# Performance work log

Hardware: AMD Instinct MI355X
Metric: run time of the kernel (lower is better)

Reference implementation:

```python
import jax, jax.numpy as jnp
import numpy as np

L, B, D, H, R, C, WIN = 256, 64, 1024, 512, 8, 6, 10
N = B * L
DH = D + H  # concat(node_features, graph output)


def _window_pairs():
    pi, pk = [], []
    for j in range(L):
        for k in range(max(0, j - WIN), min(L, j + WIN + 1)):
            pi.append(j)
            pk.append(k)
    return np.asarray(pi, np.int32), np.asarray(pk, np.int32)


def setup_inputs() -> dict:
    key = jax.random.key(0)
    ks = jax.random.split(key, 16)
    s = 0.02
    pi, pk = _window_pairs()
    return {
        "features": jax.random.normal(ks[0], (L, B, D), jnp.float32),
        "Wscalar": jax.random.normal(ks[1], (D, L), jnp.float32) * s,   # MaskedEdgeAttention scalar
        "W_rel": jax.random.normal(ks[2], (R, D, H), jnp.float32) * s,  # RGCN per-relation weights
        "W_root": jax.random.normal(ks[3], (D, H), jnp.float32) * s,
        "b_rgcn": jnp.zeros((H,), jnp.float32),
        "W_nbr": jax.random.normal(ks[4], (H, H), jnp.float32) * s,     # GraphConv neighbor weight
        "W_self": jax.random.normal(ks[5], (H, H), jnp.float32) * s,
        "b_gc": jnp.zeros((H,), jnp.float32),
        "W_match": jax.random.normal(ks[6], (DH, DH), jnp.float32) * s,  # MatchingAttention 'general2'
        "b_match": jnp.zeros((DH,), jnp.float32),
        "W_lin": jax.random.normal(ks[7], (DH, H), jnp.float32) * s,
        "b_lin": jnp.zeros((H,), jnp.float32),
        "W_fc": jax.random.normal(ks[8], (H, C), jnp.float32) * s,
        "b_fc": jnp.zeros((C,), jnp.float32),
        "speakers": jax.random.randint(ks[9], (L, B), 0, 2, jnp.int32),
        "pair_i": jnp.asarray(pi),
        "pair_k": jnp.asarray(pk),
    }


def reference(features, Wscalar, W_rel, W_root, b_rgcn, W_nbr, W_self, b_gc,
              W_match, b_match, W_lin, b_lin, W_fc, b_fc,
              speakers, pair_i, pair_k):
    # --- edge attention scores (MaskedEdgeAttention, attn1 style) ---
    scale = jnp.einsum('sbd,dm->sbm', features, Wscalar)      # [L,B,L]
    alpha = jax.nn.softmax(scale, axis=0)
    alpha = jnp.transpose(alpha, (1, 2, 0))                   # [B, anchor, src]
    win = jnp.full((L, L), 1e-10, jnp.float32).at[pair_i, pair_k].set(1.0)
    masked = alpha * win
    scores = masked / jnp.sum(masked, axis=-1, keepdims=True)  # renormalized over window
    edge_norm = scores[:, pair_i, pair_k].reshape(-1)          # [E]

    # --- batch_graphify: flatten nodes conversation-major, build global edges ---
    x = jnp.transpose(features, (1, 0, 2)).reshape(N, D)       # [N, D]
    offs = jnp.arange(B, dtype=jnp.int32)[:, None] * L
    src = (offs + pair_i[None, :]).reshape(-1)
    dst = (offs + pair_k[None, :]).reshape(-1)
    sp = speakers.T                                            # [B, L]
    dir_bit = jnp.where(pair_i < pair_k, 0, 1).astype(jnp.int32)
    rel = (sp[:, pair_i] * 4 + sp[:, pair_k] * 2 + dir_bit[None, :]).reshape(-1)

    # --- RGCNConv: per-relation transform, edge_norm-weighted sum at dst + root ---
    h_all = jnp.einsum('nd,rdh->nrh', x, W_rel)                # [N, R, H]
    msg = h_all[src, rel] * edge_norm[:, None]                 # [E, H]
    agg = jax.ops.segment_sum(msg, dst, num_segments=N)
    h1 = agg + x @ W_root + b_rgcn

    # --- GraphConv: W_nbr @ sum_j x_j + W_self @ x + b ---
    nbr = jax.ops.segment_sum(h1[src], dst, num_segments=N)
    h2 = nbr @ W_nbr + h1 @ W_self + b_gc

    # --- attentive_node_features (MatchingAttention 'general2', full-length mask=1) ---
    em = jnp.concatenate([x, h2], axis=-1).reshape(B, L, DH)
    em = jnp.transpose(em, (1, 0, 2))                          # [L, B, DH] seq-major
    xt = jnp.einsum('tbd,de->tbe', em, W_match) + b_match
    a = jax.nn.softmax(jnp.tanh(jnp.einsum('tbe,sbe->bts', xt, em)), axis=2)
    att = jnp.einsum('bts,sbd->tbd', a, em)                    # [L, B, DH]

    # --- classify_node_features (dropout = eval identity) ---
    hidden = jax.nn.relu(jnp.einsum('tbd,dh->tbh', att, W_lin) + b_lin)
    logp = jax.nn.log_softmax(hidden @ W_fc + b_fc, axis=2)    # [L, B, C]
    return jnp.transpose(logp, (1, 0, 2)).reshape(N, C)
```

## Files before the change

### kernel.cpp

```cpp
#include <hip/hip_runtime.h>
#include <hip/hip_bf16.h>

#define Lc 256
#define Bc 64
#define Dc 1024
#define Hc 512
#define Rc 8
#define Cc 6
#define WINc 10
#define NWc 21
#define Nc (Bc*Lc)
#define DHc (Dc+Hc)
#define CH 8192

typedef __attribute__((ext_vector_type(8))) short short8;
typedef __attribute__((ext_vector_type(4))) float floatx4;

__device__ inline unsigned short f2b(float x) {
    __hip_bfloat16 h = __float2bfloat16(x);
    return *reinterpret_cast<unsigned short*>(&h);
}
__device__ inline float bf2f(unsigned short u) {
    __hip_bfloat16 h;
    *reinterpret_cast<unsigned short*>(&h) = u;
    return __bfloat162float(h);
}

__device__ inline long remap_row(int node) { return (long)(((node & 255) << 6) + (node >> 8)); }

typedef __attribute__((address_space(3))) unsigned int lds_u32;
typedef __attribute__((address_space(1))) unsigned int glb_u32;
__device__ inline void glds16(const unsigned short* g, unsigned short* l) {
    __builtin_amdgcn_global_load_lds((const glb_u32*)g, (lds_u32*)l, 16, 0, 0);
}

#define SB0 __builtin_amdgcn_sched_barrier(0)
#define BAR __builtin_amdgcn_s_barrier()

__device__ __forceinline__ void xcd_remap(int gridX, int& x, int& y)
{
    int nwg = gridDim.x * gridDim.y;
    int bid = blockIdx.y * gridDim.x + blockIdx.x;
    int q = nwg >> 3, r = nwg & 7;
    int xcd = bid & 7, pos = bid >> 3;
    int logical = xcd * q + min(xcd, r) + pos;
    x = logical % gridX;
    y = logical / gridX;
}

__global__ __launch_bounds__(256) void transpose_all(
    const float* __restrict__ Wscalar, const float* __restrict__ W_rel,
    const float* __restrict__ W_root, const float* __restrict__ W_nbr,
    const float* __restrict__ W_self, const float* __restrict__ W_match,
    const float* __restrict__ W_lin, unsigned short* __restrict__ WT)
{
    int t = blockIdx.x;
    const float* in; unsigned short* out; int N, ldo, n0, k0;
    if (t < 256) {
        in = Wscalar; out = WT; N = 256; ldo = 1024;
        n0 = (t & 7) * 32; k0 = (t >> 3) * 32;
    } else if (t < 4352) {
        int u = t - 256; int r = u >> 9; u &= 511;
        in = W_rel + (long)r * 524288; out = WT + 262144 + (long)r * 524288; N = 512; ldo = 1024;
        n0 = (u & 15) * 32; k0 = (u >> 4) * 32;
    } else if (t < 4864) {
        int u = t - 4352;
        in = W_root; out = WT + 262144 + 4096 * 1024; N = 512; ldo = 1024;
        n0 = (u & 15) * 32; k0 = (u >> 4) * 32;
    } else if (t < 5120) {
        int u = t - 4864;
        in = W_nbr; out = WT + 4980736; N = 512; ldo = 1024;
        n0 = (u & 15) * 32; k0 = (u >> 4) * 32;
    } else if (t < 5376) {
        int u = t - 5120;
        in = W_self; out = WT + 4980736 + 512; N = 512; ldo = 1024;
        n0 = (u & 15) * 32; k0 = (u >> 4) * 32;
    } else if (t < 7680) {
        int u = t - 5376;
        in = W_match; out = WT + 5505024; N = 1536; ldo = 1536;
        n0 = (u % 48) * 32; k0 = (u / 48) * 32;
    } else {
        int u = t - 7680;
        in = W_lin; out = WT + 7864320; N = 512; ldo = 1536;
        n0 = (u & 15) * 32; k0 = (u >> 4) * 32;
    }
    __shared__ float tt[32][33];
    int tx = threadIdx.x & 31, ty = threadIdx.x >> 5;
    #pragma unroll
    for (int i = 0; i < 4; i++) tt[ty + i * 8][tx] = in[(long)(k0 + ty + i * 8) * N + n0 + tx];
    __syncthreads();
    #pragma unroll
    for (int i = 0; i < 4; i++) out[(long)(n0 + ty + i * 8) * ldo + k0 + tx] = f2b(tt[tx][ty + i * 8]);
}

__global__ __launch_bounds__(256) void partition_kernel(const int* __restrict__ spk,
        int* __restrict__ idx, int* __restrict__ cnts)
{
    int c = blockIdx.x;
    int tid = threadIdx.x;
    int base = c * CH;
    __shared__ int zs[256];
    int zcount = 0;
    for (int i = 0; i < CH / 256; i++) {
        int n = base + tid * (CH / 256) + i;
        if (spk[(n & 255) * 64 + (n >> 8)] == 0) zcount++;
    }
    zs[tid] = zcount; __syncthreads();
    for (int off = 1; off < 256; off <<= 1) {
        int v = (tid >= off) ? zs[tid - off] : 0;
        __syncthreads();
        zs[tid] += v;
        __syncthreads();
    }
    int Z = zs[255];
    int zpos = zs[tid] - zcount;
    int opos = tid * (CH / 256) - zpos;
    for (int i = 0; i < CH / 256; i++) {
        int nl = tid * (CH / 256) + i;
        int n = base + nl;
        if (spk[(n & 255) * 64 + (n >> 8)] == 0) idx[base + (zpos++)] = nl;
        else                                     idx[base + Z + (opos++)] = nl;
    }
    if (tid == 0) cnts[c] = Z;
}

__global__ __launch_bounds__(256) void build_em_x(const float* __restrict__ feats,
                                                  unsigned short* __restrict__ em)
{
    int n = blockIdx.x;
    int tid = threadIdx.x;
    const float* f = feats + remap_row(n) * Dc;
    float4 v = ((const float4*)f)[tid];
    unsigned short* e = em + (long)n * DHc + tid * 4;
    e[0] = f2b(v.x); e[1] = f2b(v.y); e[2] = f2b(v.z); e[3] = f2b(v.w);
}

template<bool CBF, bool CT, bool BIAS, bool RELU>
__global__ __launch_bounds__(256) void gemm_as(
    const unsigned short* __restrict__ A, const unsigned short* __restrict__ B,
    void* __restrict__ Cv, const float* __restrict__ bias,
    int K, int lda, int ldb, int ldc, long sA, long sB, long sC)
{
    __shared__ __align__(16) unsigned short As[4096];
    __shared__ __align__(16) unsigned short Bs[4096];
    const int tid = threadIdx.x;
    const int z = blockIdx.z;
    const int m0 = blockIdx.y * 128, n0 = blockIdx.x * 128;
    const int lane = tid & 63, wave = tid >> 6;
    const int q = lane >> 4, mr = lane & 15;
    const int wrow = (wave >> 1) * 64, wcol = (wave & 1) * 64;

    const unsigned short* Ag0 = A + z * sA + (long)(m0 + wave * 32 + mr) * lda + q * 8;
    const unsigned short* Ag1 = Ag0 + (long)16 * lda;
    const unsigned short* Bg0 = B + z * sB + (long)(n0 + wave * 32 + mr) * ldb + q * 8;
    const unsigned short* Bg1 = Bg0 + (long)16 * ldb;
    unsigned short* Al0 = As + wave * 1024;
    unsigned short* Bl0 = Bs + wave * 1024;

    floatx4 acc[4][4];
    #pragma unroll
    for (int mt = 0; mt < 4; mt++)
        #pragma unroll
        for (int nt = 0; nt < 4; nt++) acc[mt][nt] = (floatx4){0.f, 0.f, 0.f, 0.f};

    const int ga = (wave >> 1) * 2048;
    const int gb = (wave & 1) * 2048;

    for (int k0 = 0; k0 < K; k0 += 32) {
        glds16(Ag0 + k0, Al0);
        glds16(Ag1 + k0, Al0 + 512);
        glds16(Bg0 + k0, Bl0);
        glds16(Bg1 + k0, Bl0 + 512);
        __syncthreads();
        short8 af[4], bfr[4];
        #pragma unroll
        for (int t = 0; t < 4; t++) {
            af[t]  = *(const short8*)&As[ga + t * 512 + lane * 8];
            bfr[t] = *(const short8*)&Bs[gb + t * 512 + lane * 8];
        }
        #pragma unroll
        for (int mt = 0; mt < 4; mt++)
            #pragma unroll
            for (int nt = 0; nt < 4; nt++)
                acc[mt][nt] = __builtin_amdgcn_mfma_f32_16x16x32_bf16(af[mt], bfr[nt], acc[mt][nt], 0, 0, 0);
        __syncthreads();
    }

    float* Cf = (float*)Cv;
    unsigned short* Cb = (unsigned short*)Cv;
    #pragma unroll
    for (int mt = 0; mt < 4; mt++) {
        #pragma unroll
        for (int nt = 0; nt < 4; nt++) {
            int col = n0 + wcol + nt * 16 + mr;
            float bv = BIAS ? bias[col] : 0.f;
            #pragma unroll
            for (int rg = 0; rg < 4; rg++) {
                int row = m0 + wrow + mt * 16 + q * 4 + rg;
                float v = acc[mt][nt][rg] + bv;
                if (RELU) v = fmaxf(v, 0.f);
                if (CT) {
                    Cb[(long)(row >> 8) * 131072 + (long)col * 256 + (row & 255)] = f2b(v);
                } else {
                    long ci = z * sC + (long)row * ldc + col;
                    if (CBF) Cb[ci] = f2b(v);
                    else     Cf[ci] = v;
                }
            }
        }
    }
}

#define MFMA16(ACCBASE, AFR, BFR) \
    { _Pragma("unroll") \
      for (int mt = 0; mt < 4; mt++) \
        _Pragma("unroll") \
        for (int nt = 0; nt < 4; nt++) \
            acc[ACCBASE + mt][nt] = __builtin_amdgcn_mfma_f32_16x16x32_bf16(AFR[mt], BFR[nt], acc[ACCBASE + mt][nt], 0, 0, 0); }

__device__ __forceinline__ void gemm256_loop(
    unsigned short* lp,
    const unsigned short* Ag0, const unsigned short* Ag1,
    const unsigned short* Bg0, const unsigned short* Bg1,
    int NT, int wofs, const int* offA, const int* offB, floatx4 (&acc)[8][4])
{
    glds16(Ag0,      lp + wofs);                 glds16(Ag1,      lp + 4096 + wofs);
    glds16(Bg0,      lp + 32768 + wofs);         glds16(Bg1,      lp + 32768 + 4096 + wofs);
    glds16(Ag0 + 32, lp + 8192 + wofs);          glds16(Ag1 + 32, lp + 8192 + 4096 + wofs);
    glds16(Bg0 + 32, lp + 32768 + 8192 + wofs);  glds16(Bg1 + 32, lp + 32768 + 8192 + 4096 + wofs);
    glds16(Ag0 + 64, lp + 16384 + wofs);         glds16(Ag1 + 64, lp + 16384 + 4096 + wofs);
    glds16(Bg0 + 64, lp + 32768 + 16384 + wofs); glds16(Bg1 + 64, lp + 32768 + 16384 + 4096 + wofs);
    asm volatile("s_waitcnt vmcnt(4)" ::: "memory");
    SB0; BAR; SB0;

    short8 aQ[4], a2Q[4], bQ[4], b2Q[4];
    #pragma unroll
    for (int i = 0; i < 4; i++) aQ[i] = *(const short8*)(lp + offA[i]);
    #pragma unroll
    for (int i = 0; i < 4; i++) bQ[i] = *(const short8*)(lp + 32768 + offB[i]);

    for (int t = 0; t < NT; t++) {
        const int buf = t & 1;
        const int ab  = buf * 16384;

        if (t + 1 < NT) {
            const int kc = (t + 1) * 64 + 32;
            unsigned short* d = lp + (buf ^ 1) * 16384 + 8192 + wofs;
            glds16(Ag0 + kc, d); glds16(Ag1 + kc, d + 4096);
        }
        #pragma unroll
        for (int i = 0; i < 4; i++) a2Q[i] = *(const short8*)(lp + ab + offA[4 + i]);
        SB0; BAR; SB0;
        __builtin_amdgcn_s_setprio(1);
        MFMA16(0, aQ, bQ)
        __builtin_amdgcn_s_setprio(0);
        SB0; BAR; SB0;

        if (t + 1 < NT) {
            const int kc = (t + 1) * 64 + 32;
            unsigned short* d = lp + 32768 + (buf ^ 1) * 16384 + 8192 + wofs;
            glds16(Bg0 + kc, d); glds16(Bg1 + kc, d + 4096);
        }
        #pragma unroll
        for (int i = 0; i < 4; i++) aQ[i]  = *(const short8*)(lp + ab + 8192 + offA[i]);
        #pragma unroll
        for (int i = 0; i < 4; i++) b2Q[i] = *(const short8*)(lp + 32768 + ab + 8192 + offB[i]);
        SB0; BAR; SB0;
        __builtin_amdgcn_s_setprio(1);
        MFMA16(4, a2Q, bQ)
        __builtin_amdgcn_s_setprio(0);
        SB0; BAR; SB0;

        if (t + 2 < NT) {
            const int kc = (t + 2) * 64;
            unsigned short* d = lp + buf * 16384 + wofs;
            glds16(Ag0 + kc, d); glds16(Ag1 + kc, d + 4096);
        }
        #pragma unroll
        for (int i = 0; i < 4; i++) a2Q[i] = *(const short8*)(lp + ab + 8192 + offA[4 + i]);
        SB0; BAR; SB0;
        __builtin_amdgcn_s_setprio(1);
        MFMA16(0, aQ, b2Q)
        __builtin_amdgcn_s_setprio(0);
        SB0; BAR; SB0;

        if (t + 2 < NT) {
            const int kc = (t + 2) * 64;
            unsigned short* d = lp + 32768 + buf * 16384 + wofs;
            glds16(Bg0 + kc, d); glds16(Bg1 + kc, d + 4096);
        }
        if (t < NT - 2)       { asm volatile("s_waitcnt vmcnt(4)" ::: "memory"); }
        else if (t == NT - 2) { asm volatile("s_waitcnt vmcnt(0)" ::: "memory"); }
        SB0; BAR; SB0;
        if (t + 1 < NT) {
            const int ab2 = (buf ^ 1) * 16384;
            #pragma unroll
            for (int i = 0; i < 4; i++) aQ[i] = *(const short8*)(lp + ab2 + offA[i]);
            #pragma unroll
            for (int i = 0; i < 4; i++) bQ[i] = *(const short8*)(lp + 32768 + ab2 + offB[i]);
        }
        SB0;
        __builtin_amdgcn_s_setprio(1);
        MFMA16(4, a2Q, b2Q)
        __builtin_amdgcn_s_setprio(0);
        SB0; BAR; SB0;
    }
}

__device__ __forceinline__ void frag_offsets(int wm, int wn, int q, int mr, int* offA, int* offB)
{
    #pragma unroll
    for (int mt = 0; mt < 8; mt++) {
        int row = wm * 128 + mt * 16 + mr;
        offA[mt] = row * 32 + ((q ^ ((row >> 1) & 3)) * 8);
    }
    #pragma unroll
    for (int nt = 0; nt < 4; nt++) {
        int row = wn * 64 + nt * 16 + mr;
        offB[nt] = row * 32 + ((q ^ ((row >> 1) & 3)) * 8);
    }
}

template<bool CBF, bool CT, bool BIAS, bool RELU>
__global__ __launch_bounds__(512, 2) void gemm256(
    const unsigned short* __restrict__ A, const unsigned short* __restrict__ B,
    void* __restrict__ Cv, const float* __restrict__ bias,
    int K, int lda, int ldb, int ldc)
{
    __shared__ __align__(16) unsigned short LDS[65536];
    unsigned short* lp = &LDS[0];
    const int tid  = threadIdx.x;
    const int lane = tid & 63, wave = tid >> 6;
    const int wm = wave >> 2, wn = wave & 3;
    int bx, by;
    xcd_remap(gridDim.x, bx, by);
    const int m0 = by * 256, n0 = bx * 256;
    const int NT = K >> 6;
    const int q = lane >> 4, mr = lane & 15;

    const int r0 = wave * 16 + (lane >> 2);
    const int r1 = r0 + 128;
    const int c0 = ((lane & 3) ^ ((r0 >> 1) & 3)) * 8;
    const int c1 = ((lane & 3) ^ ((r1 >> 1) & 3)) * 8;
    const unsigned short* Ag0 = A + (long)(m0 + r0) * lda + c0;
    const unsigned short* Ag1 = A + (long)(m0 + r1) * lda + c1;
    const unsigned short* Bg0 = B + (long)(n0 + r0) * ldb + c0;
    const unsigned short* Bg1 = B + (long)(n0 + r1) * ldb + c1;
    const int wofs = wave * 512;

    int offA[8], offB[4];
    frag_offsets(wm, wn, q, mr, offA, offB);

    floatx4 acc[8][4];
    #pragma unroll
    for (int mt = 0; mt < 8; mt++)
        #pragma unroll
        for (int nt = 0; nt < 4; nt++) acc[mt][nt] = (floatx4){0.f, 0.f, 0.f, 0.f};

    gemm256_loop(lp, Ag0, Ag1, Bg0, Bg1, NT, wofs, offA, offB, acc);

    float* Cf = (float*)Cv;
    unsigned short* Cb = (unsigned short*)Cv;
    #pragma unroll
    for (int mt = 0; mt < 8; mt++) {
        #pragma unroll
        for (int nt = 0; nt < 4; nt++) {
            int col = n0 + wn * 64 + nt * 16 + mr;
            float bv = BIAS ? bias[col] : 0.f;
            #pragma unroll
            for (int rg = 0; rg < 4; rg++) {
                int row = m0 + wm * 128 + mt * 16 + q * 4 + rg;
                float v = acc[mt][nt][rg] + bv;
                if (RELU) v = fmaxf(v, 0.f);
                if (CT) {
                    Cb[(long)(row >> 8) * 131072 + (long)col * 256 + (row & 255)] = f2b(v);
                } else {
                    long ci = (long)row * ldc + col;
                    if (CBF) Cb[ci] = f2b(v);
                    else     Cf[ci] = v;
                }
            }
        }
    }
}

__global__ __launch_bounds__(512, 2) void rgcn256(
    const unsigned short* __restrict__ A, const unsigned short* __restrict__ B,
    unsigned short* __restrict__ C, const int* __restrict__ idx,
    const int* __restrict__ cntp)
{
    const int cnt0 = *cntp;
    const int t0 = (cnt0 + 255) >> 8;
    const int M1 = CH - cnt0;
    const int t1 = (M1 + 255) >> 8;
    int x, ty;
    xcd_remap(gridDim.x, x, ty);
    int sblk, m0, M, off;
    if (ty < t0)           { sblk = 0; m0 = ty << 8;        M = cnt0; off = 0; }
    else if (ty < t0 + t1) { sblk = 1; m0 = (ty - t0) << 8; M = M1;   off = cnt0; }
    else return;

    const int brow = ((x < 8) ? sblk * 2048 : 2048) + x * 256;

    __shared__ __align__(16) unsigned short LDS[65536];
    unsigned short* lp = &LDS[0];
    const int tid  = threadIdx.x;
    const int lane = tid & 63, wave = tid >> 6;
    const int wm = wave >> 2, wn = wave & 3;
    const int q = lane >> 4, mr = lane & 15;

    const int r0 = wave * 16 + (lane >> 2);
    const int r1 = r0 + 128;
    const int c0 = ((lane & 3) ^ ((r0 >> 1) & 3)) * 8;
    const int c1 = ((lane & 3) ^ ((r1 >> 1) & 3)) * 8;
    const int gr0 = idx[off + min(m0 + r0, M - 1)];
    const int gr1 = idx[off + min(m0 + r1, M - 1)];
    const unsigned short* Ag0 = A + (long)gr0 * DHc + c0;
    const unsigned short* Ag1 = A + (long)gr1 * DHc + c1;
    const unsigned short* Bg0 = B + (long)(brow + r0) * 1024 + c0;
    const unsigned short* Bg1 = B + (long)(brow + r1) * 1024 + c1;
    const int wofs = wave * 512;

    int offA[8], offB[4];
    frag_offsets(wm, wn, q, mr, offA, offB);

    floatx4 acc[8][4];
    #pragma unroll
    for (int mt = 0; mt < 8; mt++)
        #pragma unroll
        for (int nt = 0; nt < 4; nt++) acc[mt][nt] = (floatx4){0.f, 0.f, 0.f, 0.f};

    gemm256_loop(lp, Ag0, Ag1, Bg0, Bg1, 16 , wofs, offA, offB, acc);

    #pragma unroll
    for (int mt = 0; mt < 8; mt++) {
        int rowb = m0 + wm * 128 + mt * 16 + q * 4;
        int cr[4];
        #pragma unroll
        for (int rg = 0; rg < 4; rg++) cr[rg] = idx[off + min(rowb + rg, M - 1)];
        #pragma unroll
        for (int nt = 0; nt < 4; nt++) {
            int col = x * 256 + wn * 64 + nt * 16 + mr;
            #pragma unroll
            for (int rg = 0; rg < 4; rg++)
                C[(long)cr[rg] * 2560 + col] = f2b(acc[mt][nt][rg]);
        }
    }
}

__global__ __launch_bounds__(512, 2) void gemm256_mw(
    const unsigned short* __restrict__ A, const unsigned short* __restrict__ B,
    unsigned short* __restrict__ xt, unsigned short* __restrict__ emWT,
    const float* __restrict__ b_match, const float* __restrict__ b_lin)
{
    __shared__ __align__(16) unsigned short LDS[65536];
    unsigned short* lp = &LDS[0];
    const int tid  = threadIdx.x;
    const int lane = tid & 63, wave = tid >> 6;
    const int wm = wave >> 2, wn = wave & 3;
    int bx, by;
    xcd_remap(gridDim.x, bx, by);
    const int m0 = by * 256, n0 = bx * 256;
    const int q = lane >> 4, mr = lane & 15;

    const int r0 = wave * 16 + (lane >> 2);
    const int r1 = r0 + 128;
    const int c0 = ((lane & 3) ^ ((r0 >> 1) & 3)) * 8;
    const int c1 = ((lane & 3) ^ ((r1 >> 1) & 3)) * 8;
    const unsigned short* Ag0 = A + (long)(m0 + r0) * DHc + c0;
    const unsigned short* Ag1 = A + (long)(m0 + r1) * DHc + c1;
    const unsigned short* Bg0 = B + (long)(n0 + r0) * 1536 + c0;
    const unsigned short* Bg1 = B + (long)(n0 + r1) * 1536 + c1;
    const int wofs = wave * 512;

    int offA[8], offB[4];
    frag_offsets(wm, wn, q, mr, offA, offB);

    floatx4 acc[8][4];
    #pragma unroll
    for (int mt = 0; mt < 8; mt++)
        #pragma unroll
        for (int nt = 0; nt < 4; nt++) acc[mt][nt] = (floatx4){0.f, 0.f, 0.f, 0.f};

    gemm256_loop(lp, Ag0, Ag1, Bg0, Bg1, 24 , wofs, offA, offB, acc);

    if (n0 < 1536) {
        #pragma unroll
        for (int mt = 0; mt < 8; mt++) {
            #pragma unroll
            for (int nt = 0; nt < 4; nt++) {
                int col = n0 + wn * 64 + nt * 16 + mr;
                float bv = b_match[col];
                #pragma unroll
                for (int rg = 0; rg < 4; rg++) {
                    int row = m0 + wm * 128 + mt * 16 + q * 4 + rg;
                    xt[(long)row * DHc + col] = f2b(acc[mt][nt][rg] + bv);
                }
            }
        }
    } else {
        #pragma unroll
        for (int mt = 0; mt < 8; mt++) {
            #pragma unroll
            for (int nt = 0; nt < 4; nt++) {
                int col = (n0 - 1536) + wn * 64 + nt * 16 + mr;
                float bv = b_lin[col];
                #pragma unroll
                for (int rg = 0; rg < 4; rg++) {
                    int row = m0 + wm * 128 + mt * 16 + q * 4 + rg;
                    emWT[(long)(row >> 8) * 131072 + (long)col * 256 + (row & 255)] =
                        f2b(acc[mt][nt][rg] + bv);
                }
            }
        }
    }
}

__global__ __launch_bounds__(256) void edge_norm_kernel(const float* __restrict__ scale,
                                                        float* __restrict__ enorm)
{
    int g = blockIdx.x * 256 + threadIdx.x;
    int b = g >> 8, j = g & 255;
    int klo = max(0, j - WINc), khi = min(Lc - 1, j + WINc);
    float vals[NWc];
    float m = -1e30f;
    for (int k = klo; k <= khi; k++) {
        float v = scale[(long)((b << 8) + k) * Lc + j];
        vals[k - klo] = v;
        m = fmaxf(m, v);
    }
    float s = 0.f;
    for (int k = klo; k <= khi; k++) {
        float e = expf(vals[k - klo] - m);
        vals[k - klo] = e;
        s += e;
    }
    float inv = 1.f / s;
    for (int k = klo; k <= khi; k++)
        enorm[(long)g * NWc + (k - j + WINc)] = vals[k - klo] * inv;
}

__global__ __launch_bounds__(256) void rgcn_gather4(const unsigned short* __restrict__ hall4,
        const float* __restrict__ enorm, const int* __restrict__ spk,
        const float* __restrict__ b_rgcn, float* __restrict__ h1, int chunk_base)
{
    int nloc = blockIdx.x;
    int n = chunk_base + nloc;
    int b = n >> 8, k = n & 255;
    int tid = threadIdx.x;
    int spkk = spk[k * 64 + b];
    int jlo = max(0, k - WINc), jhi = min(Lc - 1, k + WINc);
    unsigned int ru = *(const unsigned int*)(hall4 + (long)nloc * 2560 + 2048 + 2 * tid);
    float a0 = bf2f((unsigned short)(ru & 0xffff)) + b_rgcn[2 * tid];
    float a1 = bf2f((unsigned short)(ru >> 16)) + b_rgcn[2 * tid + 1];
    int cb = spkk * 2;
    for (int j = jlo; j <= jhi; j++) {
        int c = cb + ((j < k) ? 0 : 1);
        float w = enorm[((long)((b << 8) + j)) * NWc + (k - j + WINc)];
        unsigned int u = *(const unsigned int*)(hall4 + ((long)(nloc - k + j)) * 2560 + c * 512 + 2 * tid);
        a0 += w * bf2f((unsigned short)(u & 0xffff));
        a1 += w * bf2f((unsigned short)(u >> 16));
    }
    *(float2*)&h1[(long)n * Hc + 2 * tid] = make_float2(a0, a1);
}

__global__ __launch_bounds__(256) void build_anh1(const float* __restrict__ h1,
                                                  unsigned short* __restrict__ anh1)
{
    int n = blockIdx.x;
    int b = n >> 8, k = n & 255;
    int tid = threadIdx.x;
    int jlo = max(0, k - WINc), jhi = min(Lc - 1, k + WINc);
    float a0 = 0.f, a1 = 0.f;
    for (int j = jlo; j <= jhi; j++) {
        const float* src = h1 + ((long)((b << 8) + j)) * Hc;
        a0 += src[tid];
        a1 += src[tid + 256];
    }
    unsigned short* dst = anh1 + (long)n * 1024;
    const float* self = h1 + (long)n * Hc;
    dst[tid]       = f2b(a0);
    dst[tid + 256] = f2b(a1);
    dst[tid + 512] = f2b(self[tid]);
    dst[tid + 768] = f2b(self[tid + 256]);
}

__global__ __launch_bounds__(256) void tanh_softmax_rows(const float* __restrict__ S,
                                                         unsigned short* __restrict__ a)
{
    int row = blockIdx.x;
    int tid = threadIdx.x;
    __shared__ float red[256];
    float v = tanhf(S[(long)row * Lc + tid]);
    red[tid] = v; __syncthreads();
    for (int s = 128; s > 0; s >>= 1) { if (tid < s) red[tid] = fmaxf(red[tid], red[tid + s]); __syncthreads(); }
    float m = red[0]; __syncthreads();
    float e = expf(v - m);
    red[tid] = e; __syncthreads();
    for (int s = 128; s > 0; s >>= 1) { if (tid < s) red[tid] += red[tid + s]; __syncthreads(); }
    float sum = red[0];
    a[(long)row * Lc + tid] = f2b(e / sum);
}

__global__ __launch_bounds__(256) void out_kernel(const unsigned short* __restrict__ hidden,
        const float* __restrict__ Wfc, const float* __restrict__ bfc, float* __restrict__ out)
{
    int tid = threadIdx.x;
    int lane = tid & 63;
    int row = blockIdx.x * 4 + (tid >> 6);
    float acc[Cc] = {};
    const unsigned short* h = hidden + (long)row * Hc;
    for (int k = lane; k < Hc; k += 64) {
        float hv = bf2f(h[k]);
        #pragma unroll
        for (int c = 0; c < Cc; c++) acc[c] += hv * Wfc[k * Cc + c];
    }
    #pragma unroll
    for (int c = 0; c < Cc; c++)
        for (int off = 32; off > 0; off >>= 1) acc[c] += __shfl_down(acc[c], off, 64);
    if (lane == 0) {
        float m = -1e30f;
        #pragma unroll
        for (int c = 0; c < Cc; c++) { acc[c] += bfc[c]; m = fmaxf(m, acc[c]); }
        float s = 0.f;
        #pragma unroll
        for (int c = 0; c < Cc; c++) s += expf(acc[c] - m);
        float lse = logf(s);
        #pragma unroll
        for (int c = 0; c < Cc; c++) out[(long)row * Cc + c] = acc[c] - m - lse;
    }
}

extern "C" void kernel_launch(void* const* d_in, const int* in_sizes, int n_in,
                              void* d_out, int out_size, void* d_ws, size_t ws_size,
                              hipStream_t stream)
{
    const float* feats   = (const float*)d_in[0];
    const float* Wscalar = (const float*)d_in[1];
    const float* W_rel   = (const float*)d_in[2];
    const float* W_root  = (const float*)d_in[3];
    const float* b_rgcn  = (const float*)d_in[4];
    const float* W_nbr   = (const float*)d_in[5];
    const float* W_self  = (const float*)d_in[6];
    const float* b_gc    = (const float*)d_in[7];
    const float* W_match = (const float*)d_in[8];
    const float* b_match = (const float*)d_in[9];
    const float* W_lin   = (const float*)d_in[10];
    const float* b_lin   = (const float*)d_in[11];
    const float* W_fc    = (const float*)d_in[12];
    const float* b_fc    = (const float*)d_in[13];
    const int*   spk     = (const int*)d_in[14];

    char* wsb = (char*)d_ws;
    unsigned short* em    = (unsigned short*)wsb;
    char* RB = wsb + 50331648;
    float*          scale = (float*)RB;
    unsigned short* hall4 = (unsigned short*)RB;
    unsigned short* anh1  = (unsigned short*)RB;
    unsigned short* xt    = (unsigned short*)RB;
    unsigned short* hidden= (unsigned short*)(RB + 16777216);
    char* HB = wsb + 100663296;
    float*          h1    = (float*)HB;
    float*          S     = (float*)HB;
    unsigned short* emWT  = (unsigned short*)(wsb + 117440512);
    int* idx              = (int*)(HB + 16777216);
    int* cnts             = (int*)(HB + 16777216 + 65536);
    unsigned short* WT    = (unsigned short*)(wsb + 134217728);
    unsigned short* WscalarT = WT;
    unsigned short* WrelT    = WT + 262144;
    unsigned short* WgcT     = WT + 4980736;
    unsigned short* WmatchT  = WT + 5505024;
    unsigned short* ac    = (unsigned short*)(wsb + 134217728);
    float*          enorm = (float*)(wsb + 151519232);

    transpose_all<<<dim3(8448), 256, 0, stream>>>(Wscalar, W_rel, W_root, W_nbr, W_self,
                                                  W_match, W_lin, WT);
    partition_kernel<<<dim3(2), 256, 0, stream>>>(spk, idx, cnts);
    build_em_x<<<dim3(Nc), 256, 0, stream>>>(feats, em);

    gemm_as<false, false, false, false><<<dim3(2, 128, 1), 256, 0, stream>>>(
        em, WscalarT, scale, nullptr, 1024, DHc, 1024, 256, 0, 0, 0);

    edge_norm_kernel<<<dim3(64), 256, 0, stream>>>(scale, enorm);

    for (int c = 0; c < 2; c++) {
        const unsigned short* emc = em + (long)c * CH * DHc;
        rgcn256<<<dim3(10, 33, 1), 512, 0, stream>>>(
            emc, WrelT, hall4, idx + c * CH, cnts + c);
        rgcn_gather4<<<dim3(CH), 256, 0, stream>>>(hall4, enorm, spk, b_rgcn, h1, c * CH);
    }

    build_anh1<<<dim3(Nc), 256, 0, stream>>>(h1, anh1);
    gemm256<true, false, true, false><<<dim3(2, 64, 1), 512, 0, stream>>>(
        anh1, WgcT, em + 1024, b_gc, 1024, 1024, 1024, DHc);

    gemm256_mw<<<dim3(8, 64, 1), 512, 0, stream>>>(
        em, WmatchT, xt, emWT, b_match, b_lin);

    gemm_as<false, false, false, false><<<dim3(2, 2, 64), 256, 0, stream>>>(
        xt, em, S, nullptr, DHc, DHc, DHc, 256, 393216, 393216, 65536);

    tanh_softmax_rows<<<dim3(Nc), 256, 0, stream>>>(S, ac);

    gemm_as<true, false, false, true><<<dim3(4, 2, 64), 256, 0, stream>>>(
        ac, emWT, hidden, nullptr, 256, 256, 256, 512, 65536, 131072, 131072);

    out_kernel<<<dim3(Nc / 4), 256, 0, stream>>>(hidden, W_fc, b_fc, (float*)d_out);
}
```

Before: 707.8 us.

## Merge prep kernels into one launch and restructure gemm256 LDS prefetch pipeline

```diff
diff --git a/kernel.cpp b/kernel.cpp
--- a/kernel.cpp
+++ b/kernel.cpp
@@ -48,13 +48,53 @@
     y = logical / gridX;
 }
 
-__global__ __launch_bounds__(256) void transpose_all(
+__global__ __launch_bounds__(256) void prep_all(
     const float* __restrict__ Wscalar, const float* __restrict__ W_rel,
     const float* __restrict__ W_root, const float* __restrict__ W_nbr,
     const float* __restrict__ W_self, const float* __restrict__ W_match,
-    const float* __restrict__ W_lin, unsigned short* __restrict__ WT)
+    const float* __restrict__ W_lin, unsigned short* __restrict__ WT,
+    const int* __restrict__ spk, int* __restrict__ idx, int* __restrict__ cnts,
+    const float* __restrict__ feats, unsigned short* __restrict__ em)
 {
     int t = blockIdx.x;
+    if (t >= 8448 + 16384) {
+        int c = t - (8448 + 16384);
+        int tid = threadIdx.x;
+        int base = c * CH;
+        __shared__ int zs[256];
+        int zcount = 0;
+        for (int i = 0; i < CH / 256; i++) {
+            int n = base + tid * (CH / 256) + i;
+            if (spk[(n & 255) * 64 + (n >> 8)] == 0) zcount++;
+        }
+        zs[tid] = zcount; __syncthreads();
+        for (int off = 1; off < 256; off <<= 1) {
+            int v = (tid >= off) ? zs[tid - off] : 0;
+            __syncthreads();
+            zs[tid] += v;
+            __syncthreads();
+        }
+        int Z = zs[255];
+        int zpos = zs[tid] - zcount;
+        int opos = tid * (CH / 256) - zpos;
+        for (int i = 0; i < CH / 256; i++) {
+            int nl = tid * (CH / 256) + i;
+            int n = base + nl;
+            if (spk[(n & 255) * 64 + (n >> 8)] == 0) idx[base + (zpos++)] = nl;
+            else                                     idx[base + Z + (opos++)] = nl;
+        }
+        if (tid == 0) cnts[c] = Z;
+        return;
+    }
+    if (t >= 8448) {
+        int n = t - 8448;
+        int tid = threadIdx.x;
+        const float* f = feats + remap_row(n) * Dc;
+        float4 v = ((const float4*)f)[tid];
+        unsigned short* e = em + (long)n * DHc + tid * 4;
+        e[0] = f2b(v.x); e[1] = f2b(v.y); e[2] = f2b(v.z); e[3] = f2b(v.w);
+        return;
+    }
     const float* in; unsigned short* out; int N, ldo, n0, k0;
     if (t < 256) {
         in = Wscalar; out = WT; N = 256; ldo = 1024;
@@ -93,48 +133,6 @@
     for (int i = 0; i < 4; i++) out[(long)(n0 + ty + i * 8) * ldo + k0 + tx] = f2b(tt[tx][ty + i * 8]);
 }
 
-__global__ __launch_bounds__(256) void partition_kernel(const int* __restrict__ spk,
-        int* __restrict__ idx, int* __restrict__ cnts)
-{
-    int c = blockIdx.x;
-    int tid = threadIdx.x;
-    int base = c * CH;
-    __shared__ int zs[256];
-    int zcount = 0;
-    for (int i = 0; i < CH / 256; i++) {
-        int n = base + tid * (CH / 256) + i;
-        if (spk[(n & 255) * 64 + (n >> 8)] == 0) zcount++;
-    }
-    zs[tid] = zcount; __syncthreads();
-    for (int off = 1; off < 256; off <<= 1) {
-        int v = (tid >= off) ? zs[tid - off] : 0;
-        __syncthreads();
-        zs[tid] += v;
-        __syncthreads();
-    }
-    int Z = zs[255];
-    int zpos = zs[tid] - zcount;
-    int opos = tid * (CH / 256) - zpos;
-    for (int i = 0; i < CH / 256; i++) {
-        int nl = tid * (CH / 256) + i;
-        int n = base + nl;
-        if (spk[(n & 255) * 64 + (n >> 8)] == 0) idx[base + (zpos++)] = nl;
-        else                                     idx[base + Z + (opos++)] = nl;
-    }
-    if (tid == 0) cnts[c] = Z;
-}
-
-__global__ __launch_bounds__(256) void build_em_x(const float* __restrict__ feats,
-                                                  unsigned short* __restrict__ em)
-{
-    int n = blockIdx.x;
-    int tid = threadIdx.x;
-    const float* f = feats + remap_row(n) * Dc;
-    float4 v = ((const float4*)f)[tid];
-    unsigned short* e = em + (long)n * DHc + tid * 4;
-    e[0] = f2b(v.x); e[1] = f2b(v.y); e[2] = f2b(v.z); e[3] = f2b(v.w);
-}
-
 template<bool CBF, bool CT, bool BIAS, bool RELU>
 __global__ __launch_bounds__(256) void gemm_as(
     const unsigned short* __restrict__ A, const unsigned short* __restrict__ B,
@@ -224,84 +222,82 @@
     const unsigned short* Bg0, const unsigned short* Bg1,
     int NT, int wofs, const int* offA, const int* offB, floatx4 (&acc)[8][4])
 {
-    glds16(Ag0,      lp + wofs);                 glds16(Ag1,      lp + 4096 + wofs);
-    glds16(Bg0,      lp + 32768 + wofs);         glds16(Bg1,      lp + 32768 + 4096 + wofs);
-    glds16(Ag0 + 32, lp + 8192 + wofs);          glds16(Ag1 + 32, lp + 8192 + 4096 + wofs);
-    glds16(Bg0 + 32, lp + 32768 + 8192 + wofs);  glds16(Bg1 + 32, lp + 32768 + 8192 + 4096 + wofs);
-    glds16(Ag0 + 64, lp + 16384 + wofs);         glds16(Ag1 + 64, lp + 16384 + 4096 + wofs);
-    glds16(Bg0 + 64, lp + 32768 + 16384 + wofs); glds16(Bg1 + 64, lp + 32768 + 16384 + 4096 + wofs);
-    asm volatile("s_waitcnt vmcnt(4)" ::: "memory");
+    unsigned short* Bl = lp + 32768;
+    glds16(Ag0,      lp + wofs);                glds16(Ag1,      lp + wofs + 4096);
+    glds16(Ag0 + 32, lp + 8192 + wofs);         glds16(Ag1 + 32, lp + 8192 + wofs + 4096);
+    glds16(Bg0,      Bl + wofs);                glds16(Bg1,      Bl + wofs + 4096);
+    glds16(Bg0 + 32, Bl + 8192 + wofs);         glds16(Bg1 + 32, Bl + 8192 + wofs + 4096);
+    glds16(Bg0 + 64, Bl + 16384 + wofs);        glds16(Bg1 + 64, Bl + 16384 + wofs + 4096);
+    glds16(Bg0 + 96, Bl + 16384 + 8192 + wofs); glds16(Bg1 + 96, Bl + 16384 + 8192 + wofs + 4096);
+    glds16(Ag0 + 64, lp + 16384 + wofs);        glds16(Ag1 + 64, lp + 16384 + wofs + 4096);
+    asm volatile("s_waitcnt vmcnt(6)" ::: "memory");
     SB0; BAR; SB0;
 
-    short8 aQ[4], a2Q[4], bQ[4], b2Q[4];
-    #pragma unroll
-    for (int i = 0; i < 4; i++) aQ[i] = *(const short8*)(lp + offA[i]);
-    #pragma unroll
-    for (int i = 0; i < 4; i++) bQ[i] = *(const short8*)(lp + 32768 + offB[i]);
-
+    short8 aF[4], bQ[4], b2Q[4];
     for (int t = 0; t < NT; t++) {
         const int buf = t & 1;
         const int ab  = buf * 16384;
-
+        const int abx = (buf ^ 1) * 16384;
+
+        #pragma unroll
+        for (int i = 0; i < 4; i++) aF[i] = *(const short8*)(lp + ab + offA[i]);
+        #pragma unroll
+        for (int i = 0; i < 4; i++) bQ[i] = *(const short8*)(Bl + ab + offB[i]);
         if (t + 1 < NT) {
             const int kc = (t + 1) * 64 + 32;
-            unsigned short* d = lp + (buf ^ 1) * 16384 + 8192 + wofs;
-            glds16(Ag0 + kc, d); glds16(Ag1 + kc, d + 4096);
-        }
-        #pragma unroll
-        for (int i = 0; i < 4; i++) a2Q[i] = *(const short8*)(lp + ab + offA[4 + i]);
+            glds16(Ag0 + kc, lp + abx + 8192 + wofs);
+            glds16(Ag1 + kc, lp + abx + 8192 + wofs + 4096);
+        }
         SB0; BAR; SB0;
+        asm volatile("s_waitcnt lgkmcnt(0)" ::: "memory"); SB0;
         __builtin_amdgcn_s_setprio(1);
-        MFMA16(0, aQ, bQ)
+        MFMA16(0, aF, bQ)
         __builtin_amdgcn_s_setprio(0);
         SB0; BAR; SB0;
 
-        if (t + 1 < NT) {
-            const int kc = (t + 1) * 64 + 32;
-            unsigned short* d = lp + 32768 + (buf ^ 1) * 16384 + 8192 + wofs;
-            glds16(Bg0 + kc, d); glds16(Bg1 + kc, d + 4096);
-        }
-        #pragma unroll
-        for (int i = 0; i < 4; i++) aQ[i]  = *(const short8*)(lp + ab + 8192 + offA[i]);
-        #pragma unroll
-        for (int i = 0; i < 4; i++) b2Q[i] = *(const short8*)(lp + 32768 + ab + 8192 + offB[i]);
+        #pragma unroll
+        for (int i = 0; i < 4; i++) aF[i]  = *(const short8*)(lp + ab + offA[4 + i]);
+        #pragma unroll
+        for (int i = 0; i < 4; i++) b2Q[i] = *(const short8*)(Bl + ab + 8192 + offB[i]);
+        if (t + 2 < NT) {
+            const int kc = (t + 2) * 64;
+            glds16(Bg0 + kc, Bl + ab + wofs);
+            glds16(Bg1 + kc, Bl + ab + wofs + 4096);
+        }
         SB0; BAR; SB0;
+        asm volatile("s_waitcnt lgkmcnt(0)" ::: "memory"); SB0;
         __builtin_amdgcn_s_setprio(1);
-        MFMA16(4, a2Q, bQ)
+        MFMA16(4, aF, bQ)
         __builtin_amdgcn_s_setprio(0);
         SB0; BAR; SB0;
 
+        #pragma unroll
+        for (int i = 0; i < 4; i++) aF[i] = *(const short8*)(lp + ab + 8192 + offA[i]);
+        if (t + 2 < NT) {
+            const int kc = (t + 2) * 64 + 32;
+            glds16(Bg0 + kc, Bl + ab + 8192 + wofs);
+            glds16(Bg1 + kc, Bl + ab + 8192 + wofs + 4096);
+        }
+        SB0; BAR; SB0;
+        asm volatile("s_waitcnt lgkmcnt(0)" ::: "memory"); SB0;
+        __builtin_amdgcn_s_setprio(1);
+        MFMA16(0, aF, b2Q)
+        __builtin_amdgcn_s_setprio(0);
+        SB0; BAR; SB0;
+
+        #pragma unroll
+        for (int i = 0; i < 4; i++) aF[i] = *(const short8*)(lp + ab + 8192 + offA[4 + i]);
         if (t + 2 < NT) {
             const int kc = (t + 2) * 64;
-            unsigned short* d = lp + buf * 16384 + wofs;
-            glds16(Ag0 + kc, d); glds16(Ag1 + kc, d + 4096);
-        }
-        #pragma unroll
-        for (int i = 0; i < 4; i++) a2Q[i] = *(const short8*)(lp + ab + 8192 + offA[4 + i]);
-        SB0; BAR; SB0;
-        __builtin_amdgcn_s_setprio(1);
-        MFMA16(0, aQ, b2Q)
-        __builtin_amdgcn_s_setprio(0);
-        SB0; BAR; SB0;
-
-        if (t + 2 < NT) {
-            const int kc = (t + 2) * 64;
-            unsigned short* d = lp + 32768 + buf * 16384 + wofs;
-            glds16(Bg0 + kc, d); glds16(Bg1 + kc, d + 4096);
-        }
-        if (t < NT - 2)       { asm volatile("s_waitcnt vmcnt(4)" ::: "memory"); }
+            glds16(Ag0 + kc, lp + ab + wofs);
+            glds16(Ag1 + kc, lp + ab + wofs + 4096);
+        }
+        if (t < NT - 2)       { asm volatile("s_waitcnt vmcnt(6)" ::: "memory"); }
         else if (t == NT - 2) { asm volatile("s_waitcnt vmcnt(0)" ::: "memory"); }
         SB0; BAR; SB0;
-        if (t + 1 < NT) {
-            const int ab2 = (buf ^ 1) * 16384;
-            #pragma unroll
-            for (int i = 0; i < 4; i++) aQ[i] = *(const short8*)(lp + ab2 + offA[i]);
-            #pragma unroll
-            for (int i = 0; i < 4; i++) bQ[i] = *(const short8*)(lp + 32768 + ab2 + offB[i]);
-        }
-        SB0;
+        asm volatile("s_waitcnt lgkmcnt(0)" ::: "memory"); SB0;
         __builtin_amdgcn_s_setprio(1);
-        MFMA16(4, a2Q, b2Q)
+        MFMA16(4, aF, b2Q)
         __builtin_amdgcn_s_setprio(0);
         SB0; BAR; SB0;
     }
@@ -673,10 +669,9 @@
     unsigned short* ac    = (unsigned short*)(wsb + 134217728);
     float*          enorm = (float*)(wsb + 151519232);
 
-    transpose_all<<<dim3(8448), 256, 0, stream>>>(Wscalar, W_rel, W_root, W_nbr, W_self,
-                                                  W_match, W_lin, WT);
-    partition_kernel<<<dim3(2), 256, 0, stream>>>(spk, idx, cnts);
-    build_em_x<<<dim3(Nc), 256, 0, stream>>>(feats, em);
+    prep_all<<<dim3(8448 + 16384 + 2), 256, 0, stream>>>(
+        Wscalar, W_rel, W_root, W_nbr, W_self, W_match, W_lin, WT,
+        spk, idx, cnts, feats, em);
 
     gemm_as<false, false, false, false><<<dim3(2, 128, 1), 256, 0, stream>>>(
         em, WscalarT, scale, nullptr, 1024, DHc, 1024, 256, 0, 0, 0);
```

Result: no change. 704.2 us (-0.5%).
